# Performance work log

Hardware: AMD Instinct MI355X
Metric: run time of the kernel (lower is better)

Reference implementation:

```python
import jax, jax.numpy as jnp
from jax import lax
import numpy as np


def _conv1d(x, w, b):
    # x: (N, C, L), w: (O, I, K), stride 2, padding 1 -> matches nn.Conv1d(k=4, s=2, p=1)
    y = lax.conv_general_dilated(x, w, window_strides=(2,), padding=[(1, 1)],
                                 dimension_numbers=('NCH', 'OIH', 'NCH'))
    return y + b[None, :, None]


def setup_inputs() -> dict:
    key = jax.random.key(0)
    k = jax.random.split(key, 6)
    B, C_in, T = 32, 256, 2048
    H, D, K_codes = 1024, 512, 1024
    s = 0.02
    return {
        'x': jax.random.normal(k[0], (B, C_in, T), dtype=jnp.float32),
        'w1': jax.random.normal(k[1], (H, C_in, 4), dtype=jnp.float32) * s,
        'b1': jnp.zeros((H,), dtype=jnp.float32),
        'w2': jax.random.normal(k[2], (D, H, 4), dtype=jnp.float32) * s,
        'b2': jnp.zeros((D,), dtype=jnp.float32),
        'codebook': jax.random.normal(k[3], (K_codes, D), dtype=jnp.float32) * s,
    }


def reference(x, w1, b1, w2, b2, codebook):
    z_e = _conv1d(jax.nn.relu(_conv1d(x, w1, b1)), w2, b2)  # (B, D, T/4)
    B, D, T = z_e.shape
    flat = z_e.transpose(0, 2, 1).reshape(-1, D)  # (B*T, D)
    # squared Euclidean distance; argmin identical to cdist(p=2) argmin
    d2 = (jnp.sum(flat * flat, axis=1, keepdims=True)
          - 2.0 * flat @ codebook.T
          + jnp.sum(codebook * codebook, axis=1)[None, :])  # (B*T, K)
    encoding_indices = jnp.argmin(d2, axis=1)  # (B*T,)
    # NOTE: faithful to the original .view(z_e.shape) (a raw reshape, no permute back)
    z_q = codebook[encoding_indices].reshape(B, D, T)
    return (z_q, encoding_indices, z_e)
```

## Files before the change

kernel.cpp:

```cpp
#include <hip/hip_runtime.h>
#include <hip/hip_bf16.h>

using f16x8 = __attribute__((ext_vector_type(8))) _Float16;
using f32x4 = __attribute__((ext_vector_type(4))) float;

union PackU { unsigned u; _Float16 h[2]; };

__device__ inline unsigned split_pack(float v) {
    _Float16 h0 = (_Float16)v;
    float r = (v - (float)h0) * 4096.0f;
    PackU p; p.h[0] = h0; p.h[1] = (_Float16)r;
    return p.u;
}

__global__ __launch_bounds__(256) void split_kernel(const float* __restrict__ src,
                                                    unsigned* __restrict__ dst, int n4) {
    int g = blockIdx.x * 256 + threadIdx.x;
    if (g >= n4) return;
    float4 v = reinterpret_cast<const float4*>(src)[g];
    uint4 o;
    o.x = split_pack(v.x); o.y = split_pack(v.y);
    o.z = split_pack(v.z); o.w = split_pack(v.w);
    reinterpret_cast<uint4*>(dst)[g] = o;
}

#define BMt 128
#define BNt 128
#define BKt 32

__global__ __launch_bounds__(256, 2) void mfma_gemm(
    const unsigned* __restrict__ Ap, const unsigned* __restrict__ Bp,
    const float* __restrict__ bias,
    unsigned* __restrict__ OutP, float* __restrict__ OutF,
    int M, int N, int KK, int Cc, int L, int Lout, int LoutSh,
    int gatherMode, int mode)
{
    __shared__ uint4 As4[BMt * 8];
    __shared__ uint4 Bs4[BNt * 8];

    const int tid = threadIdx.x;
    const int m0 = blockIdx.y * BMt;
    const int n0 = blockIdx.x * BNt;

    const int srow = tid >> 1;
    const int kh = tid & 1;
    const int am = m0 + srow;
    const int ab = am >> LoutSh;
    const int at = am & (Lout - 1);
    const unsigned* aprow = Ap + (size_t)ab * Cc * L;
    const int ai0 = 2 * at - 1;
    const unsigned* adir = Ap + (size_t)am * KK;
    const unsigned* brow = Bp + (size_t)(n0 + srow) * KK;

    const int lane = tid & 63;
    const int wv = tid >> 6;
    const int wr = wv >> 1, wc = wv & 1;
    const int l15 = lane & 15, lq = lane >> 4;

    f32x4 acc0[4][4] = {{{0.f}}};
    f32x4 acc1[4][4] = {{{0.f}}};

    for (int k0 = 0; k0 < KK; k0 += BKt) {
        uint4 pa[4], pb[4];
        if (gatherMode) {
            int cbase = (k0 >> 2) + kh * 4;
#pragma unroll
            for (int cl = 0; cl < 4; cl++) {
                const unsigned* base = aprow + (size_t)(cbase + cl) * L;
                unsigned q0 = 0, q3 = 0;
                if (ai0 >= 0) q0 = base[ai0];
                unsigned q1 = base[ai0 + 1];
                unsigned q2 = base[ai0 + 2];
                if (ai0 + 3 < L) q3 = base[ai0 + 3];
                pa[cl].x = q0; pa[cl].y = q1; pa[cl].z = q2; pa[cl].w = q3;
            }
        } else {
            const uint4* s = reinterpret_cast<const uint4*>(adir + k0 + kh * 16);
            pa[0] = s[0]; pa[1] = s[1]; pa[2] = s[2]; pa[3] = s[3];
        }
        {
            const uint4* s = reinterpret_cast<const uint4*>(brow + k0 + kh * 16);
            pb[0] = s[0]; pb[1] = s[1]; pb[2] = s[2]; pb[3] = s[3];
        }

        __syncthreads();

#pragma unroll
        for (int ch = 0; ch < 2; ch++) {
            uint4 w0, w1, v0, v1;
            unsigned* W0 = (unsigned*)&w0; unsigned* W1 = (unsigned*)&w1;
            unsigned* V0 = (unsigned*)&v0; unsigned* V1 = (unsigned*)&v1;
#pragma unroll
            for (int j = 0; j < 4; j++) {
                int e0 = ch * 8 + 2 * j, e1 = e0 + 1;
                unsigned lo = ((const unsigned*)&pa[e0 >> 2])[e0 & 3];
                unsigned hi = ((const unsigned*)&pa[e1 >> 2])[e1 & 3];
                W0[j] = __builtin_amdgcn_perm(hi, lo, 0x05040100u);
                W1[j] = __builtin_amdgcn_perm(hi, lo, 0x07060302u);
                lo = ((const unsigned*)&pb[e0 >> 2])[e0 & 3];
                hi = ((const unsigned*)&pb[e1 >> 2])[e1 & 3];
                V0[j] = __builtin_amdgcn_perm(hi, lo, 0x05040100u);
                V1[j] = __builtin_amdgcn_perm(hi, lo, 0x07060302u);
            }
            int kc = kh * 2 + ch;
            int sw = srow & 7;
            As4[srow * 8 + ((kc) ^ sw)] = w0;
            As4[srow * 8 + ((4 + kc) ^ sw)] = w1;
            Bs4[srow * 8 + ((kc) ^ sw)] = v0;
            Bs4[srow * 8 + ((4 + kc) ^ sw)] = v1;
        }

        __syncthreads();

        f16x8 a0f[4], a1f[4], b0f[4], b1f[4];
#pragma unroll
        for (int mf = 0; mf < 4; mf++) {
            int row = wr * 64 + mf * 16 + l15;
            int sw = row & 7;
            a0f[mf] = *reinterpret_cast<const f16x8*>(&As4[row * 8 + (lq ^ sw)]);
            a1f[mf] = *reinterpret_cast<const f16x8*>(&As4[row * 8 + ((4 + lq) ^ sw)]);
        }
#pragma unroll
        for (int nf = 0; nf < 4; nf++) {
            int row = wc * 64 + nf * 16 + l15;
            int sw = row & 7;
            b0f[nf] = *reinterpret_cast<const f16x8*>(&Bs4[row * 8 + (lq ^ sw)]);
            b1f[nf] = *reinterpret_cast<const f16x8*>(&Bs4[row * 8 + ((4 + lq) ^ sw)]);
        }
#pragma unroll
        for (int mf = 0; mf < 4; mf++)
#pragma unroll
            for (int nf = 0; nf < 4; nf++) {
                acc0[mf][nf] = __builtin_amdgcn_mfma_f32_16x16x32_f16(
                    a0f[mf], b0f[nf], acc0[mf][nf], 0, 0, 0);
                acc1[mf][nf] = __builtin_amdgcn_mfma_f32_16x16x32_f16(
                    a0f[mf], b1f[nf], acc1[mf][nf], 0, 0, 0);
                acc1[mf][nf] = __builtin_amdgcn_mfma_f32_16x16x32_f16(
                    a1f[mf], b0f[nf], acc1[mf][nf], 0, 0, 0);
            }
    }

    const float s12 = 1.0f / 4096.0f;
    const int LoutM = Lout - 1;

    if (mode == 2) {
#pragma unroll
        for (int mf = 0; mf < 4; mf++) {
            int mb = m0 + wr * 64 + mf * 16 + lq * 4;
#pragma unroll
            for (int nf = 0; nf < 4; nf++) {
                int n = n0 + wc * 64 + nf * 16 + l15;
#pragma unroll
                for (int r = 0; r < 4; r++) {
                    float v = acc0[mf][nf][r] + acc1[mf][nf][r] * s12;
                    OutF[(size_t)(mb + r) * N + n] = v;
                }
            }
        }
    } else if (mode == 0) {
#pragma unroll
        for (int mf = 0; mf < 4; mf++) {
            int mb = m0 + wr * 64 + mf * 16 + lq * 4;
            int b = mb >> LoutSh, t = mb & LoutM;
#pragma unroll
            for (int nf = 0; nf < 4; nf++) {
                int n = n0 + wc * 64 + nf * 16 + l15;
                float bv = bias[n];
                uint4 o;
                unsigned* O = (unsigned*)&o;
#pragma unroll
                for (int r = 0; r < 4; r++) {
                    float v = acc0[mf][nf][r] + acc1[mf][nf][r] * s12 + bv;
                    v = fmaxf(v, 0.f);
                    O[r] = split_pack(v);
                }
                *reinterpret_cast<uint4*>(&OutP[((size_t)b * N + n) * Lout + t]) = o;
            }
        }
    } else {
#pragma unroll
        for (int mf = 0; mf < 4; mf++) {
            int mb = m0 + wr * 64 + mf * 16 + lq * 4;
            int b = mb >> LoutSh, t = mb & LoutM;
#pragma unroll
            for (int nf = 0; nf < 4; nf++) {
                int n = n0 + wc * 64 + nf * 16 + l15;
                float bv = bias[n];
                float4 f;
                unsigned O[4];
#pragma unroll
                for (int r = 0; r < 4; r++) {
                    float v = acc0[mf][nf][r] + acc1[mf][nf][r] * s12 + bv;
                    ((float*)&f)[r] = v;
                    O[r] = split_pack(v);
                }
                *reinterpret_cast<float4*>(&OutF[((size_t)b * N + n) * Lout + t]) = f;
#pragma unroll
                for (int r = 0; r < 4; r++)
                    OutP[(size_t)(mb + r) * N + n] = O[r];
            }
        }
    }
}

__global__ __launch_bounds__(64) void cb_norm(const float* __restrict__ cb,
                                              float* __restrict__ cn2) {
    int n = blockIdx.x;
    int lane = threadIdx.x;
    float s = 0.f;
    for (int d = lane; d < 512; d += 64) {
        float v = cb[(size_t)n * 512 + d];
        s += v * v;
    }
#pragma unroll
    for (int off = 32; off; off >>= 1) s += __shfl_down(s, off);
    if (lane == 0) cn2[n] = s;
}

__global__ __launch_bounds__(256) void argmin_k(const float* __restrict__ S,
                                                const float* __restrict__ cn2,
                                                float* __restrict__ idxf,
                                                int* __restrict__ idxi, int rows) {
    int wid = threadIdx.x >> 6;
    int lane = threadIdx.x & 63;
    int r = blockIdx.x * 4 + wid;
    if (r >= rows) return;
    const float* srow = S + (size_t)r * 1024;
    float best = INFINITY;
    int bi = 0;
#pragma unroll
    for (int it = 0; it < 4; it++) {
        int nb = it * 256 + lane * 4;
        float4 s4 = *reinterpret_cast<const float4*>(&srow[nb]);
        float4 c4 = *reinterpret_cast<const float4*>(&cn2[nb]);
        float v;
        v = c4.x - 2.f * s4.x; if (v < best) { best = v; bi = nb + 0; }
        v = c4.y - 2.f * s4.y; if (v < best) { best = v; bi = nb + 1; }
        v = c4.z - 2.f * s4.z; if (v < best) { best = v; bi = nb + 2; }
        v = c4.w - 2.f * s4.w; if (v < best) { best = v; bi = nb + 3; }
    }
#pragma unroll
    for (int off = 32; off; off >>= 1) {
        float ov = __shfl_down(best, off);
        int oi = __shfl_down(bi, off);
        if (ov < best || (ov == best && oi < bi)) { best = ov; bi = oi; }
    }
    if (lane == 0) {
        idxf[r] = (float)bi;
        idxi[r] = bi;
    }
}

__global__ __launch_bounds__(256) void gather_k(const int* __restrict__ idx,
                                                const float* __restrict__ cb,
                                                float* __restrict__ zq, int total4) {
    int g = blockIdx.x * 256 + threadIdx.x;
    if (g >= total4) return;
    int r = g >> 7;
    int d4 = g & 127;
    int id = idx[r];
    *reinterpret_cast<float4*>(&zq[(size_t)r * 512 + (size_t)d4 * 4]) =
        *reinterpret_cast<const float4*>(&cb[(size_t)id * 512 + (size_t)d4 * 4]);
}

extern "C" void kernel_launch(void* const* d_in, const int* in_sizes, int n_in,
                              void* d_out, int out_size, void* d_ws, size_t ws_size,
                              hipStream_t stream) {
    const float* x  = (const float*)d_in[0];
    const float* w1 = (const float*)d_in[1];
    const float* b1 = (const float*)d_in[2];
    const float* w2 = (const float*)d_in[3];
    const float* b2 = (const float*)d_in[4];
    const float* cb = (const float*)d_in[5];
    float* out = (float*)d_out;

    const int B = 32, Cin = 256, T = 2048, H = 1024, D = 512, Kc = 1024;
    const int T1 = 1024, T2 = 512;

    float* zq_out  = out;
    float* idx_out = out + (size_t)B * T2 * D;
    float* ze_out  = idx_out + (size_t)B * T2;

    unsigned* w1p = (unsigned*)d_ws;
    unsigned* w2p = w1p + (size_t)H * Cin * 4;
    unsigned* cbp = w2p + (size_t)D * H * 4;
    float* cn2    = (float*)(cbp + (size_t)Kc * D);
    int* idx_ws   = (int*)(cn2 + Kc);
    unsigned* dyn = (unsigned*)(idx_ws + B * T2);

    size_t fixed_u32 = (size_t)H * Cin * 4 + (size_t)D * H * 4 + (size_t)Kc * D
                       + Kc + (size_t)B * T2 + 256;
    int NB = 32;
    while (NB > 1 &&
           (fixed_u32 + (size_t)NB * ((size_t)Cin * T + (size_t)H * T1 + (size_t)T2 * D))
               * 4 > ws_size)
        NB >>= 1;

    unsigned* xp = dyn;
    unsigned* hp = xp + (size_t)NB * Cin * T;
    unsigned* zp = hp + (size_t)NB * H * T1;
    float* S = (float*)hp;

    split_kernel<<<(H * Cin * 4 / 4 + 255) / 256, 256, 0, stream>>>(w1, w1p, H * Cin * 4 / 4);
    split_kernel<<<(D * H * 4 / 4 + 255) / 256, 256, 0, stream>>>(w2, w2p, D * H * 4 / 4);
    split_kernel<<<(Kc * D / 4 + 255) / 256, 256, 0, stream>>>(cb, cbp, Kc * D / 4);
    cb_norm<<<Kc, 64, 0, stream>>>(cb, cn2);

    for (int b0 = 0; b0 < B; b0 += NB) {
        int nb = (B - b0 < NB) ? (B - b0) : NB;

        split_kernel<<<(nb * Cin * T / 4 + 255) / 256, 256, 0, stream>>>(
            x + (size_t)b0 * Cin * T, xp, nb * Cin * T / 4);

        mfma_gemm<<<dim3(H / BNt, nb * T1 / BMt), 256, 0, stream>>>(
            xp, w1p, b1, hp, nullptr,
            nb * T1, H, Cin * 4, Cin, T, T1, 10, 1, 0);

        mfma_gemm<<<dim3(D / BNt, nb * T2 / BMt), 256, 0, stream>>>(
            hp, w2p, b2, zp, ze_out + (size_t)b0 * D * T2,
            nb * T2, D, H * 4, H, T1, T2, 9, 1, 1);

        mfma_gemm<<<dim3(Kc / BNt, nb * T2 / BMt), 256, 0, stream>>>(
            zp, cbp, nullptr, nullptr, S,
            nb * T2, Kc, D, D, T2, T2, 9, 0, 2);

        argmin_k<<<(nb * T2 + 3) / 4, 256, 0, stream>>>(
            S, cn2, idx_out + (size_t)b0 * T2, idx_ws, nb * T2);

        gather_k<<<(nb * T2 * D / 4 + 255) / 256, 256, 0, stream>>>(
            idx_ws, cb, zq_out + (size_t)b0 * T2 * D, nb * T2 * D / 4);
    }
}
```

Measured before the change: 618.1 us.

## Double-buffer shared-memory tiles and prefetch next K-tile during MFMA compute

Shared memory for the A and B tiles becomes double-buffered. Each iteration now issues the global loads for the next tile before computing on the current one and writes them to the alternate buffer afterwards, so one barrier per iteration replaces two and global latency overlaps the MFMAs. B fragments are now loaded per column fragment inside the compute loop rather than all up front, which lowers register pressure. The cost is twice the LDS footprint, which may reduce occupancy, and prefetch registers that stay live across the compute.

```diff
diff --git a/kernel.cpp b/kernel.cpp
--- a/kernel.cpp
+++ b/kernel.cpp
@@ -35,8 +35,8 @@
     int M, int N, int KK, int Cc, int L, int Lout, int LoutSh,
     int gatherMode, int mode)
 {
-    __shared__ uint4 As4[BMt * 8];
-    __shared__ uint4 Bs4[BNt * 8];
+    __shared__ uint4 As4[2][BMt * 8];
+    __shared__ uint4 Bs4[2][BNt * 8];
 
     const int tid = threadIdx.x;
     const int m0 = blockIdx.y * BMt;
@@ -44,6 +44,7 @@
 
     const int srow = tid >> 1;
     const int kh = tid & 1;
+    const int sw_s = srow & 7;
     const int am = m0 + srow;
     const int ab = am >> LoutSh;
     const int at = am & (Lout - 1);
@@ -60,8 +61,9 @@
     f32x4 acc0[4][4] = {{{0.f}}};
     f32x4 acc1[4][4] = {{{0.f}}};
 
-    for (int k0 = 0; k0 < KK; k0 += BKt) {
-        uint4 pa[4], pb[4];
+    uint4 pa[4], pb[4];
+
+    auto loadT = [&](int k0) {
         if (gatherMode) {
             int cbase = (k0 >> 2) + kh * 4;
 #pragma unroll
@@ -78,13 +80,11 @@
             const uint4* s = reinterpret_cast<const uint4*>(adir + k0 + kh * 16);
             pa[0] = s[0]; pa[1] = s[1]; pa[2] = s[2]; pa[3] = s[3];
         }
-        {
-            const uint4* s = reinterpret_cast<const uint4*>(brow + k0 + kh * 16);
-            pb[0] = s[0]; pb[1] = s[1]; pb[2] = s[2]; pb[3] = s[3];
-        }
-
-        __syncthreads();
-
+        const uint4* s = reinterpret_cast<const uint4*>(brow + k0 + kh * 16);
+        pb[0] = s[0]; pb[1] = s[1]; pb[2] = s[2]; pb[3] = s[3];
+    };
+
+    auto stage = [&](int buf) {
 #pragma unroll
         for (int ch = 0; ch < 2; ch++) {
             uint4 w0, w1, v0, v1;
@@ -103,41 +103,50 @@
                 V1[j] = __builtin_amdgcn_perm(hi, lo, 0x07060302u);
             }
             int kc = kh * 2 + ch;
-            int sw = srow & 7;
-            As4[srow * 8 + ((kc) ^ sw)] = w0;
-            As4[srow * 8 + ((4 + kc) ^ sw)] = w1;
-            Bs4[srow * 8 + ((kc) ^ sw)] = v0;
-            Bs4[srow * 8 + ((4 + kc) ^ sw)] = v1;
-        }
+            As4[buf][srow * 8 + ((kc) ^ sw_s)] = w0;
+            As4[buf][srow * 8 + ((4 + kc) ^ sw_s)] = w1;
+            Bs4[buf][srow * 8 + ((kc) ^ sw_s)] = v0;
+            Bs4[buf][srow * 8 + ((4 + kc) ^ sw_s)] = v1;
+        }
+    };
+
+    const int NT = KK / BKt;
+
+    loadT(0);
+    stage(0);
+
+    for (int kt = 0; kt < NT; kt++) {
+        const int cur = kt & 1;
+        if (kt + 1 < NT) loadT((kt + 1) * BKt);
 
         __syncthreads();
 
-        f16x8 a0f[4], a1f[4], b0f[4], b1f[4];
+        f16x8 a0f[4], a1f[4];
 #pragma unroll
         for (int mf = 0; mf < 4; mf++) {
             int row = wr * 64 + mf * 16 + l15;
             int sw = row & 7;
-            a0f[mf] = *reinterpret_cast<const f16x8*>(&As4[row * 8 + (lq ^ sw)]);
-            a1f[mf] = *reinterpret_cast<const f16x8*>(&As4[row * 8 + ((4 + lq) ^ sw)]);
+            a0f[mf] = *reinterpret_cast<const f16x8*>(&As4[cur][row * 8 + (lq ^ sw)]);
+            a1f[mf] = *reinterpret_cast<const f16x8*>(&As4[cur][row * 8 + ((4 + lq) ^ sw)]);
         }
 #pragma unroll
         for (int nf = 0; nf < 4; nf++) {
             int row = wc * 64 + nf * 16 + l15;
             int sw = row & 7;
-            b0f[nf] = *reinterpret_cast<const f16x8*>(&Bs4[row * 8 + (lq ^ sw)]);
-            b1f[nf] = *reinterpret_cast<const f16x8*>(&Bs4[row * 8 + ((4 + lq) ^ sw)]);
-        }
-#pragma unroll
-        for (int mf = 0; mf < 4; mf++)
-#pragma unroll
-            for (int nf = 0; nf < 4; nf++) {
+            f16x8 b0f = *reinterpret_cast<const f16x8*>(&Bs4[cur][row * 8 + (lq ^ sw)]);
+            f16x8 b1f = *reinterpret_cast<const f16x8*>(&Bs4[cur][row * 8 + ((4 + lq) ^ sw)]);
+#pragma unroll
+            for (int mf = 0; mf < 4; mf++) {
                 acc0[mf][nf] = __builtin_amdgcn_mfma_f32_16x16x32_f16(
-                    a0f[mf], b0f[nf], acc0[mf][nf], 0, 0, 0);
+                    a0f[mf], b0f, acc0[mf][nf], 0, 0, 0);
                 acc1[mf][nf] = __builtin_amdgcn_mfma_f32_16x16x32_f16(
-                    a0f[mf], b1f[nf], acc1[mf][nf], 0, 0, 0);
+                    a0f[mf], b1f, acc1[mf][nf], 0, 0, 0);
                 acc1[mf][nf] = __builtin_amdgcn_mfma_f32_16x16x32_f16(
-                    a1f[mf], b0f[nf], acc1[mf][nf], 0, 0, 0);
-            }
+                    a1f[mf], b0f, acc1[mf][nf], 0, 0, 0);
+            }
+        }
+
+        if (kt + 1 < NT) stage(cur ^ 1);
     }
 
     const float s12 = 1.0f / 4096.0f;
```

Result: faster. 580.7 us (-6.0%).
